# Kernel optimization log

Measured on AMD Instinct MI355X. Metric: run time of the kernel, lower is better.

The kernel has to match this reference:

```python
import jax, jax.numpy as jnp
import numpy as np

N_NODES = 100000


def gcn_conv(x, edge_index, edge_weight, W, b):
    """PyG GCNConv: out = D^-1/2 (A + I) D^-1/2 X W + b (self-loop weight 1)."""
    n = x.shape[0]
    src, dst = edge_index[0], edge_index[1]
    loop = jnp.arange(n)
    src_sl = jnp.concatenate([src, loop])
    dst_sl = jnp.concatenate([dst, loop])
    ew_sl = jnp.concatenate([edge_weight, jnp.ones((n,), x.dtype)])
    deg = jax.ops.segment_sum(ew_sl, dst_sl, num_segments=n)  # [N]
    dinv = jnp.where(deg > 0, jax.lax.rsqrt(deg), 0.0)
    norm = dinv[src_sl] * ew_sl * dinv[dst_sl]  # [E+N]
    h = x @ W  # [N, out_dim] dense transform before propagation
    msg = h[src_sl] * norm[:, None]  # gather + scale, [E+N, out_dim]
    out = jax.ops.segment_sum(msg, dst_sl, num_segments=n)  # scatter-add
    return out + b


def setup_inputs() -> dict:
    key = jax.random.key(0)
    ks = jax.random.split(key, 9)
    in_dim, hidden, latent = 128, 64, 32
    n, e = N_NODES, 1600000
    x = jax.random.normal(ks[0], (n, in_dim), dtype=jnp.float32)
    edge_index = jax.random.randint(ks[1], (2, e), 0, n, dtype=jnp.int64)
    edge_weight = jax.random.uniform(ks[2], (e,), dtype=jnp.float32)
    def glorot(k, fan_in, fan_out):
        s = jnp.sqrt(6.0 / (fan_in + fan_out))
        return jax.random.uniform(k, (fan_in, fan_out), jnp.float32, -s, s)
    return {
        "x": x,
        "edge_index": edge_index,
        "edge_weight": edge_weight,
        "W1": glorot(ks[3], in_dim, hidden),
        "b1": jnp.zeros((hidden,), jnp.float32),
        "W_mu": glorot(ks[4], hidden, latent),
        "b_mu": jnp.zeros((latent,), jnp.float32),
        "W_lv": glorot(ks[5], hidden, latent),
        "b_lv": jnp.zeros((latent,), jnp.float32),
    }


def reference(x, edge_index, edge_weight, W1, b1, W_mu, b_mu, W_lv, b_lv):
    h = jax.nn.relu(gcn_conv(x, edge_index, edge_weight, W1, b1))
    mu = gcn_conv(h, edge_index, edge_weight, W_mu, b_mu)
    logvar = gcn_conv(h, edge_index, edge_weight, W_lv, b_lv)
    return (mu, logvar)
```

## Files before the change

kernel.cpp:

```cpp
#include <hip/hip_runtime.h>

static __device__ __forceinline__ float4 ld4(const float* p) { return *(const float4*)p; }
static __device__ __forceinline__ float b2f(unsigned short u) {
    return __uint_as_float((unsigned)u << 16);
}
static __device__ __forceinline__ float b2f_lo(unsigned u) { return __uint_as_float(u << 16); }
static __device__ __forceinline__ float b2f_hi(unsigned u) { return __uint_as_float(u & 0xFFFF0000u); }
static __device__ __forceinline__ unsigned short f2b(float f) {
    unsigned x = __float_as_uint(f);
    return (unsigned short)((x + 0x7FFFu + ((x >> 16) & 1u)) >> 16);
}
static __device__ __forceinline__ unsigned pk2(float lo, float hi) {
    return (unsigned)f2b(lo) | ((unsigned)f2b(hi) << 16);
}

typedef __attribute__((ext_vector_type(8))) short bf16x8;
typedef __attribute__((ext_vector_type(4))) float f32x4;

#define NPB 256
#define CAPE 5120



__global__ __launch_bounds__(256) void k_prep(const float* __restrict__ W1,
                                              const float* __restrict__ Wmu,
                                              const float* __restrict__ Wlv,
                                              unsigned short* __restrict__ Wf1,
                                              unsigned short* __restrict__ Wf2) {
    int tid = threadIdx.x;
    if (blockIdx.x == 0) {
        for (int idx = tid; idx < 2048; idx += 256) {
            int frag = idx >> 6, lane = idx & 63;
            int s = frag & 1, ct = (frag >> 1) & 3, kb = frag >> 3;
            int rA = lane & 15, g8 = (lane >> 4) * 8;
            int c = ct * 16 + rA;
            unsigned short* dstp = Wf1 + frag * 512 + lane * 8;
            for (int j = 0; j < 8; j++) {
                float wv = W1[(size_t)(kb * 32 + g8 + j) * 64 + c];
                unsigned short hi = f2b(wv);
                dstp[j] = (s == 0) ? hi : f2b(wv - b2f(hi));
            }
        }
    } else {
        for (int idx = tid; idx < 1024; idx += 256) {
            int frag = idx >> 6, lane = idx & 63;
            int s = frag & 1, ct = (frag >> 1) & 3, kb = frag >> 3;
            int rA = lane & 15, g8 = (lane >> 4) * 8;
            int c = ct * 16 + rA;
            int k0 = kb * 32 + g8;
            unsigned short* dstp = Wf2 + frag * 512 + lane * 8;
            for (int j = 0; j < 8; j++) {
                float wv = (c < 32) ? Wmu[(size_t)(k0 + j) * 32 + c]
                                    : Wlv[(size_t)(k0 + j) * 32 + (c - 32)];
                unsigned short hi = f2b(wv);
                dstp[j] = (s == 0) ? hi : f2b(wv - b2f(hi));
            }
        }
    }
}

static __device__ __forceinline__ void split8(const float* xv, bf16x8& ah, bf16x8& al) {
    #pragma unroll
    for (int j = 0; j < 8; j++) {
        unsigned u = __float_as_uint(xv[j]);
        float res = xv[j] - __uint_as_float(u & 0xFFFF0000u);
        ah[j] = (short)(u >> 16);
        al[j] = (short)(__float_as_uint(res) >> 16);
    }
}

__global__ __launch_bounds__(256) void k_fused1(const float* __restrict__ A,
                                                const unsigned short* __restrict__ Wf1,
                                                unsigned short* __restrict__ gout,
                                                const int* __restrict__ src,
                                                const int* __restrict__ dst,
                                                const float* __restrict__ ew,
                                                int* __restrict__ bin_cnt,
                                                unsigned long long* __restrict__ ebuf,
                                                int n, int E, int gb, int bb_cnt, int NB) {
    __shared__ int hist[512];
    __shared__ int hbase[512];
    int tid = threadIdx.x;
    int bid = blockIdx.x;

    if ((bid % 5) != 4) {
        int gi = (bid / 5) * 4 + (bid % 5);
        if (gi >= gb) return;
        int row0 = gi * 64;
        int w = tid >> 6, lane = tid & 63;
        int rA = lane & 15, g8 = (lane >> 4) * 8;
        int row = row0 + w * 16 + rA;
        const float* xr = A + (size_t)min(row, n - 1) * 128;
        f32x4 acc[4] = {{0.f,0.f,0.f,0.f},{0.f,0.f,0.f,0.f},{0.f,0.f,0.f,0.f},{0.f,0.f,0.f,0.f}};
        float4 c0 = ld4(xr + g8);
        float4 c1 = ld4(xr + g8 + 4);
        #pragma unroll
        for (int kb = 0; kb < 4; kb++) {
            float4 n0, n1;
            if (kb < 3) {
                n0 = ld4(xr + (kb + 1) * 32 + g8);
                n1 = ld4(xr + (kb + 1) * 32 + g8 + 4);
            }
            float xv[8] = {c0.x, c0.y, c0.z, c0.w, c1.x, c1.y, c1.z, c1.w};
            bf16x8 ah, al;
            split8(xv, ah, al);
            const unsigned short* wb = Wf1 + (size_t)(kb * 8) * 512 + lane * 8;
            #pragma unroll
            for (int ct = 0; ct < 4; ct++) {
                bf16x8 bh = *(const bf16x8*)(wb + (ct * 2 + 0) * 512);
                bf16x8 bl = *(const bf16x8*)(wb + (ct * 2 + 1) * 512);
                acc[ct] = __builtin_amdgcn_mfma_f32_16x16x32_bf16(ah, bh, acc[ct], 0, 0, 0);
                acc[ct] = __builtin_amdgcn_mfma_f32_16x16x32_bf16(al, bh, acc[ct], 0, 0, 0);
                acc[ct] = __builtin_amdgcn_mfma_f32_16x16x32_bf16(ah, bl, acc[ct], 0, 0, 0);
            }
            if (kb < 3) { c0 = n0; c1 = n1; }
        }
        int rbase = row0 + w * 16 + (lane >> 4) * 4;
        #pragma unroll
        for (int reg = 0; reg < 4; reg++) {
            int grow = rbase + reg;
            if (grow < n) {
                #pragma unroll
                for (int ct = 0; ct < 4; ct++)
                    gout[(size_t)grow * 64 + ct * 16 + rA] = f2b(acc[ct][reg]);
            }
        }
    } else {
        int bi = bid / 5;
        if (bi >= bb_cnt) return;
        for (int j = tid; j < NB; j += 256) hist[j] = 0;
        __syncthreads();
        int e0 = bi * 4096;
        unsigned long long pk[16]; int bb[16]; int loc[16];
        #pragma unroll
        for (int j = 0; j < 16; j++) {
            int e = e0 + j * 256 + tid;
            if (e < E) {
                int s = src[e];
                int d = dst[e];
                float w = ew[e];
                bb[j] = d >> 8;
                pk[j] = ((unsigned long long)__float_as_uint(w) << 32) |
                        (unsigned)((d & (NPB - 1)) << 17) | (unsigned)s;
                loc[j] = atomicAdd(&hist[bb[j]], 1);
            } else bb[j] = -1;
        }
        __syncthreads();
        for (int j = tid; j < NB; j += 256) hbase[j] = atomicAdd(&bin_cnt[j], hist[j]);
        __syncthreads();
        #pragma unroll
        for (int j = 0; j < 16; j++) {
            if (bb[j] >= 0)
                ebuf[(size_t)bb[j] * CAPE + hbase[bb[j]] + loc[j]] = pk[j];
        }
    }
}

__global__ __launch_bounds__(512) void k_csr_build(const unsigned long long* __restrict__ ebuf,
                                                   const int* __restrict__ bin_cnt,
                                                   int2* __restrict__ rowcnt,
                                                   float* __restrict__ dinv,
                                                   unsigned long long* __restrict__ csr,
                                                   int n) {
    __shared__ unsigned long long eL[CAPE];
    __shared__ unsigned cntL[NPB];
    __shared__ unsigned ewsL[NPB];
    __shared__ unsigned fillL[NPB];
    __shared__ int scanL[512];
    __shared__ int rowL[NPB];
    __shared__ int binbase_s;
    int b = blockIdx.x;
    int tid = threadIdx.x;
    if (tid < NPB) { cntL[tid] = 0; ewsL[tid] = 0; fillL[tid] = 0; }
    scanL[tid] = (tid < b) ? bin_cnt[tid] : 0;
    __syncthreads();
    int m = bin_cnt[b];
    const unsigned long long* eb = ebuf + (size_t)b * CAPE;
    for (int i = tid; i < m; i += 512) {
        unsigned long long pk = eb[i];
        eL[i] = pk;
        int ld = (int)((pk >> 17) & (NPB - 1));
        float w = __uint_as_float((unsigned)(pk >> 32));
        atomicAdd(&cntL[ld], 1u);
        atomicAdd(&ewsL[ld], (unsigned)(w * 16777216.0f));
    }
    __syncthreads();
    #pragma unroll
    for (int off = 256; off > 0; off >>= 1) {
        if (tid < off) scanL[tid] += scanL[tid + off];
        __syncthreads();
    }
    if (tid == 0) binbase_s = scanL[0];
    __syncthreads();
    int v = (tid < NPB) ? (int)cntL[tid] : 0;
    scanL[tid] = v;
    __syncthreads();
    #pragma unroll
    for (int off = 1; off < 512; off <<= 1) {
        int t = (tid >= off) ? scanL[tid - off] : 0;
        __syncthreads();
        scanL[tid] += t;
        __syncthreads();
    }
    if (tid < NPB) {
        int rp = binbase_s + scanL[tid] - v;
        rowL[tid] = rp;
        int node = b * NPB + tid;
        if (node < n) {
            rowcnt[node] = make_int2(rp, v);
            dinv[node] = rsqrtf(1.0f + (float)ewsL[tid] * (1.0f / 16777216.0f));
        }
    }
    __syncthreads();
    for (int i = tid; i < m; i += 512) {
        unsigned long long pk = eL[i];
        int s = (int)(pk & 0x1FFFF);
        int ld = (int)((pk >> 17) & (NPB - 1));
        int pos = rowL[ld] + (int)atomicAdd(&fillL[ld], 1u);
        csr[pos] = (unsigned long long)(unsigned)s | (pk & 0xFFFFFFFF00000000ull);
    }
}

__global__ __launch_bounds__(256) void k_gemm2(const unsigned short* __restrict__ h,
                                               const unsigned short* __restrict__ Wf2,
                                               const float* __restrict__ dinv,
                                               unsigned short* __restrict__ out, int n) {
    int tid = threadIdx.x;
    int row0 = blockIdx.x * 128;
    int w = tid >> 6, lane = tid & 63;
    int rA = lane & 15, g8 = (lane >> 4) * 8;
    int rowa = row0 + w * 16 + rA;
    int rowb = rowa + 64;
    const unsigned short* ha = h + (size_t)min(rowa, n - 1) * 64;
    const unsigned short* hb = h + (size_t)min(rowb, n - 1) * 64;
    f32x4 acc0[4] = {{0.f,0.f,0.f,0.f},{0.f,0.f,0.f,0.f},{0.f,0.f,0.f,0.f},{0.f,0.f,0.f,0.f}};
    f32x4 acc1[4] = {{0.f,0.f,0.f,0.f},{0.f,0.f,0.f,0.f},{0.f,0.f,0.f,0.f},{0.f,0.f,0.f,0.f}};
    #pragma unroll
    for (int kb = 0; kb < 2; kb++) {
        bf16x8 aA = *(const bf16x8*)(ha + kb * 32 + g8);
        bf16x8 aB = *(const bf16x8*)(hb + kb * 32 + g8);
        const unsigned short* wb = Wf2 + (size_t)(kb * 8) * 512 + lane * 8;
        #pragma unroll
        for (int ct = 0; ct < 4; ct++) {
            bf16x8 bh = *(const bf16x8*)(wb + (ct * 2 + 0) * 512);
            bf16x8 bl = *(const bf16x8*)(wb + (ct * 2 + 1) * 512);
            acc0[ct] = __builtin_amdgcn_mfma_f32_16x16x32_bf16(aA, bh, acc0[ct], 0, 0, 0);
            acc0[ct] = __builtin_amdgcn_mfma_f32_16x16x32_bf16(aA, bl, acc0[ct], 0, 0, 0);
            acc1[ct] = __builtin_amdgcn_mfma_f32_16x16x32_bf16(aB, bh, acc1[ct], 0, 0, 0);
            acc1[ct] = __builtin_amdgcn_mfma_f32_16x16x32_bf16(aB, bl, acc1[ct], 0, 0, 0);
        }
    }
    int rbase = row0 + w * 16 + (lane >> 4) * 4;
    #pragma unroll
    for (int reg = 0; reg < 4; reg++) {
        int grow = rbase + reg;
        if (grow < n) {
            float sc = dinv[grow];
            #pragma unroll
            for (int ct = 0; ct < 4; ct++)
                out[(size_t)grow * 64 + ct * 16 + rA] = f2b(acc0[ct][reg] * sc);
        }
        int grow2 = grow + 64;
        if (grow2 < n) {
            float sc = dinv[grow2];
            #pragma unroll
            for (int ct = 0; ct < 4; ct++)
                out[(size_t)grow2 * 64 + ct * 16 + rA] = f2b(acc1[ct][reg] * sc);
        }
    }
}

static __device__ __forceinline__ void acc8(float* a, uint4 r, float wt) {
    a[0] = fmaf(b2f_lo(r.x), wt, a[0]); a[1] = fmaf(b2f_hi(r.x), wt, a[1]);
    a[2] = fmaf(b2f_lo(r.y), wt, a[2]); a[3] = fmaf(b2f_hi(r.y), wt, a[3]);
    a[4] = fmaf(b2f_lo(r.z), wt, a[4]); a[5] = fmaf(b2f_hi(r.z), wt, a[5]);
    a[6] = fmaf(b2f_lo(r.w), wt, a[6]); a[7] = fmaf(b2f_hi(r.w), wt, a[7]);
}

template<bool RELU, bool SPLIT_OUT, bool DSCALE>
__global__ __launch_bounds__(256) void k_prop(const unsigned short* __restrict__ g,
                                              const int2* __restrict__ csr,
                                              const int2* __restrict__ rowcnt,
                                              const float* __restrict__ dinv,
                                              const float* __restrict__ bias0,
                                              const float* __restrict__ bias1,
                                              void* __restrict__ outv, int n) {
    int node = blockIdx.x * 4 + (threadIdx.x >> 6);
    if (node >= n) return;
    int lane = threadIdx.x & 63;
    int q = lane >> 3;
    int t = lane & 7;
    uint4 sr = *(const uint4*)(g + (size_t)node * 64 + t * 8);
    int2 rc = rowcnt[node];
    const int2* ep = csr + rc.x;
    int m = rc.y;
    float a[8] = {};
    if (m > 0 && m <= 16) {
        int e1 = q, e2 = q + 8;
        int i1 = min(e1, m - 1), i2 = min(e2, m - 1);
        int2 p1 = ep[i1];
        int2 p2 = ep[i2];
        uint4 r1 = *(const uint4*)(g + (size_t)p1.x * 64 + t * 8);
        uint4 r2 = *(const uint4*)(g + (size_t)p2.x * 64 + t * 8);
        float w1 = (e1 < m) ? __int_as_float(p1.y) : 0.f;
        float w2 = (e2 < m) ? __int_as_float(p2.y) : 0.f;
        if (DSCALE) { w1 *= dinv[p1.x]; w2 *= dinv[p2.x]; }
        acc8(a, r1, w1);
        acc8(a, r2, w2);
    } else {
        for (int e = 0; e < m; e += 32) {
            int e1 = e + q, e2 = e1 + 8, e3 = e1 + 16, e4 = e1 + 24;
            int i1 = min(e1, m - 1), i2 = min(e2, m - 1);
            int i3 = min(e3, m - 1), i4 = min(e4, m - 1);
            int2 p1 = ep[i1];
            int2 p2 = ep[i2];
            int2 p3 = ep[i3];
            int2 p4 = ep[i4];
            uint4 r1 = *(const uint4*)(g + (size_t)p1.x * 64 + t * 8);
            uint4 r2 = *(const uint4*)(g + (size_t)p2.x * 64 + t * 8);
            uint4 r3 = *(const uint4*)(g + (size_t)p3.x * 64 + t * 8);
            uint4 r4 = *(const uint4*)(g + (size_t)p4.x * 64 + t * 8);
            float w1 = (e1 < m) ? __int_as_float(p1.y) : 0.f;
            float w2 = (e2 < m) ? __int_as_float(p2.y) : 0.f;
            float w3 = (e3 < m) ? __int_as_float(p3.y) : 0.f;
            float w4 = (e4 < m) ? __int_as_float(p4.y) : 0.f;
            if (DSCALE) {
                w1 *= dinv[p1.x]; w2 *= dinv[p2.x];
                w3 *= dinv[p3.x]; w4 *= dinv[p4.x];
            }
            acc8(a, r1, w1);
            acc8(a, r2, w2);
            acc8(a, r3, w3);
            acc8(a, r4, w4);
        }
    }
    #pragma unroll
    for (int i = 0; i < 8; i++) {
        a[i] += __shfl_xor(a[i], 8);
        a[i] += __shfl_xor(a[i], 16);
        a[i] += __shfl_xor(a[i], 32);
    }
    if (q != 0) return;
    float di = dinv[node];
    float ss = DSCALE ? di : 1.f;
    a[0] += ss * b2f_lo(sr.x); a[1] += ss * b2f_hi(sr.x);
    a[2] += ss * b2f_lo(sr.y); a[3] += ss * b2f_hi(sr.y);
    a[4] += ss * b2f_lo(sr.z); a[5] += ss * b2f_hi(sr.z);
    a[6] += ss * b2f_lo(sr.w); a[7] += ss * b2f_hi(sr.w);
    #pragma unroll
    for (int i = 0; i < 8; i++) a[i] *= di;
    if (!SPLIT_OUT) {
        float4 b0 = ld4(bias0 + t * 8);
        float4 b1 = ld4(bias0 + t * 8 + 4);
        a[0] += b0.x; a[1] += b0.y; a[2] += b0.z; a[3] += b0.w;
        a[4] += b1.x; a[5] += b1.y; a[6] += b1.z; a[7] += b1.w;
        if (RELU) {
            #pragma unroll
            for (int i = 0; i < 8; i++) a[i] = fmaxf(a[i], 0.f);
        }
        uint4 u = make_uint4(pk2(a[0], a[1]), pk2(a[2], a[3]),
                             pk2(a[4], a[5]), pk2(a[6], a[7]));
        *(uint4*)((unsigned short*)outv + (size_t)node * 64 + t * 8) = u;
    } else {
        float* out = (float*)outv;
        const float* bp = (t < 4) ? (bias0 + t * 8) : (bias1 + (t - 4) * 8);
        size_t base = (t < 4) ? ((size_t)node * 32 + t * 8)
                              : ((size_t)n * 32 + (size_t)node * 32 + (t - 4) * 8);
        float4 b0 = ld4(bp);
        float4 b1 = ld4(bp + 4);
        float4 v0 = make_float4(a[0] + b0.x, a[1] + b0.y, a[2] + b0.z, a[3] + b0.w);
        float4 v1 = make_float4(a[4] + b1.x, a[5] + b1.y, a[6] + b1.z, a[7] + b1.w);
        *(float4*)&out[base] = v0;
        *(float4*)&out[base + 4] = v1;
    }
}

extern "C" void kernel_launch(void* const* d_in, const int* in_sizes, int n_in,
                              void* d_out, int out_size, void* d_ws, size_t ws_size,
                              hipStream_t stream) {
    const float* x   = (const float*)d_in[0];
    const int*   ei  = (const int*)d_in[1];
    const float* ew  = (const float*)d_in[2];
    const float* W1  = (const float*)d_in[3];
    const float* b1  = (const float*)d_in[4];
    const float* Wmu = (const float*)d_in[5];
    const float* bmu = (const float*)d_in[6];
    const float* Wlv = (const float*)d_in[7];
    const float* blv = (const float*)d_in[8];
    float* outp = (float*)d_out;

    const int n = in_sizes[0] / 128;
    const int E = in_sizes[2];
    const int* src = ei;
    const int* dst = ei + E;
    const int NB = (n + NPB - 1) / NPB;

    size_t o = 0;
    auto alloc = [&](size_t bytes) { void* p = (char*)d_ws + o; o += (bytes + 511) & ~(size_t)511; return p; };
    int*   bin_cnt  = (int*)alloc((size_t)NB * 4);
    int2*  rowcnt   = (int2*)alloc((size_t)n * 8);
    float* dinv     = (float*)alloc((size_t)n * 4);
    unsigned long long* csr  = (unsigned long long*)alloc((size_t)E * 8);
    unsigned long long* ebuf = (unsigned long long*)alloc((size_t)NB * CAPE * 8);
    unsigned short* g0 = (unsigned short*)alloc((size_t)n * 64 * 2);
    unsigned short* h  = (unsigned short*)alloc((size_t)n * 64 * 2);
    unsigned short* Wf1 = (unsigned short*)alloc(32 * 512 * 2);
    unsigned short* Wf2 = (unsigned short*)alloc(16 * 512 * 2);
    unsigned short* g2 = g0;

    const int gb = (n + 63) / 64;
    const int bb = (E + 4095) / 4096;
    const int groups = max(bb, (gb + 3) / 4);

    k_prep<<<2, 256, 0, stream>>>(W1, Wmu, Wlv, Wf1, Wf2);
    hipMemsetAsync(bin_cnt, 0, (size_t)NB * 4, stream);
    k_fused1<<<groups * 5, 256, 0, stream>>>(x, Wf1, g0, src, dst, ew,
                                             bin_cnt, ebuf, n, E, gb, bb, NB);
    k_csr_build<<<NB, 512, 0, stream>>>(ebuf, bin_cnt, rowcnt, dinv, csr, n);
    k_prop<true, false, true><<<(n + 3) / 4, 256, 0, stream>>>(g0, (const int2*)csr, rowcnt, dinv,
                                                               b1, nullptr, h, n);
    k_gemm2<<<(n + 127) / 128, 256, 0, stream>>>(h, Wf2, dinv, g2, n);
    k_prop<false, true, false><<<(n + 3) / 4, 256, 0, stream>>>(g2, (const int2*)csr, rowcnt, dinv,
                                                                bmu, blv, outp, n);
}
```

Measured before the change: 274.1 us.

## Build CSR via global atomic degree count, block scan and atomic scatter

Replaces the binned edge buffer and per-bin shared-memory CSR build with three steps. A global 64-bit atomic per edge packs each node's degree count and fixed-point weight sum into one word. A per-block scan then assigns row bases through an atomic counter. A scatter kernel places edges using atomic fill counters. The source-side dinv is folded into the stored edge weight, so the propagation kernels and gemm2 no longer load or apply dinv per neighbour. This trades shared-memory binning for uncoalesced global atomics and random CSR writes, and rows end up in arbitrary block order.

Result: slower. 393.4 us (+43.5%).

```diff
diff --git a/kernel.cpp b/kernel.cpp
--- a/kernel.cpp
+++ b/kernel.cpp
@@ -16,9 +16,6 @@
 
 typedef __attribute__((ext_vector_type(8))) short bf16x8;
 typedef __attribute__((ext_vector_type(4))) float f32x4;
-
-#define NPB 256
-#define CAPE 5120
 
 
 
@@ -72,21 +69,15 @@
 __global__ __launch_bounds__(256) void k_fused1(const float* __restrict__ A,
                                                 const unsigned short* __restrict__ Wf1,
                                                 unsigned short* __restrict__ gout,
-                                                const int* __restrict__ src,
                                                 const int* __restrict__ dst,
                                                 const float* __restrict__ ew,
-                                                int* __restrict__ bin_cnt,
-                                                unsigned long long* __restrict__ ebuf,
-                                                int n, int E, int gb, int bb_cnt, int NB) {
-    __shared__ int hist[512];
-    __shared__ int hbase[512];
+                                                unsigned long long* __restrict__ deg,
+                                                int n, int E, int gb) {
     int tid = threadIdx.x;
     int bid = blockIdx.x;
 
-    if ((bid % 5) != 4) {
-        int gi = (bid / 5) * 4 + (bid % 5);
-        if (gi >= gb) return;
-        int row0 = gi * 64;
+    if (bid < gb) {
+        int row0 = bid * 64;
         int w = tid >> 6, lane = tid & 63;
         int rA = lane & 15, g8 = (lane >> 4) * 8;
         int row = row0 + w * 16 + rA;
@@ -126,104 +117,71 @@
             }
         }
     } else {
-        int bi = bid / 5;
-        if (bi >= bb_cnt) return;
-        for (int j = tid; j < NB; j += 256) hist[j] = 0;
-        __syncthreads();
-        int e0 = bi * 4096;
-        unsigned long long pk[16]; int bb[16]; int loc[16];
+        int e0 = (bid - gb) * 4096;
         #pragma unroll
         for (int j = 0; j < 16; j++) {
             int e = e0 + j * 256 + tid;
             if (e < E) {
-                int s = src[e];
                 int d = dst[e];
-                float w = ew[e];
-                bb[j] = d >> 8;
-                pk[j] = ((unsigned long long)__float_as_uint(w) << 32) |
-                        (unsigned)((d & (NPB - 1)) << 17) | (unsigned)s;
-                loc[j] = atomicAdd(&hist[bb[j]], 1);
-            } else bb[j] = -1;
-        }
-        __syncthreads();
-        for (int j = tid; j < NB; j += 256) hbase[j] = atomicAdd(&bin_cnt[j], hist[j]);
-        __syncthreads();
-        #pragma unroll
-        for (int j = 0; j < 16; j++) {
-            if (bb[j] >= 0)
-                ebuf[(size_t)bb[j] * CAPE + hbase[bb[j]] + loc[j]] = pk[j];
-        }
-    }
-}
-
-__global__ __launch_bounds__(512) void k_csr_build(const unsigned long long* __restrict__ ebuf,
-                                                   const int* __restrict__ bin_cnt,
-                                                   int2* __restrict__ rowcnt,
-                                                   float* __restrict__ dinv,
-                                                   unsigned long long* __restrict__ csr,
-                                                   int n) {
-    __shared__ unsigned long long eL[CAPE];
-    __shared__ unsigned cntL[NPB];
-    __shared__ unsigned ewsL[NPB];
-    __shared__ unsigned fillL[NPB];
-    __shared__ int scanL[512];
-    __shared__ int rowL[NPB];
-    __shared__ int binbase_s;
-    int b = blockIdx.x;
+                unsigned wfix = (unsigned)(ew[e] * 16777216.0f);
+                atomicAdd(&deg[d], (1ull << 32) | (unsigned long long)wfix);
+            }
+        }
+    }
+}
+
+__global__ __launch_bounds__(256) void k_rowptr(const unsigned long long* __restrict__ deg,
+                                                int2* __restrict__ rowcnt,
+                                                float* __restrict__ dinv,
+                                                int* __restrict__ fill,
+                                                int* __restrict__ ctr, int n) {
+    __shared__ int scanL[256];
+    __shared__ int gbase_s;
     int tid = threadIdx.x;
-    if (tid < NPB) { cntL[tid] = 0; ewsL[tid] = 0; fillL[tid] = 0; }
-    scanL[tid] = (tid < b) ? bin_cnt[tid] : 0;
+    int node = blockIdx.x * 256 + tid;
+    unsigned long long dv = (node < n) ? deg[node] : 0ull;
+    int c = (int)(dv >> 32);
+    scanL[tid] = c;
     __syncthreads();
-    int m = bin_cnt[b];
-    const unsigned long long* eb = ebuf + (size_t)b * CAPE;
-    for (int i = tid; i < m; i += 512) {
-        unsigned long long pk = eb[i];
-        eL[i] = pk;
-        int ld = (int)((pk >> 17) & (NPB - 1));
-        float w = __uint_as_float((unsigned)(pk >> 32));
-        atomicAdd(&cntL[ld], 1u);
-        atomicAdd(&ewsL[ld], (unsigned)(w * 16777216.0f));
-    }
-    __syncthreads();
-    #pragma unroll
-    for (int off = 256; off > 0; off >>= 1) {
-        if (tid < off) scanL[tid] += scanL[tid + off];
-        __syncthreads();
-    }
-    if (tid == 0) binbase_s = scanL[0];
-    __syncthreads();
-    int v = (tid < NPB) ? (int)cntL[tid] : 0;
-    scanL[tid] = v;
-    __syncthreads();
-    #pragma unroll
-    for (int off = 1; off < 512; off <<= 1) {
+    #pragma unroll
+    for (int off = 1; off < 256; off <<= 1) {
         int t = (tid >= off) ? scanL[tid - off] : 0;
         __syncthreads();
         scanL[tid] += t;
         __syncthreads();
     }
-    if (tid < NPB) {
-        int rp = binbase_s + scanL[tid] - v;
-        rowL[tid] = rp;
-        int node = b * NPB + tid;
-        if (node < n) {
-            rowcnt[node] = make_int2(rp, v);
-            dinv[node] = rsqrtf(1.0f + (float)ewsL[tid] * (1.0f / 16777216.0f));
-        }
-    }
+    if (tid == 255) gbase_s = atomicAdd(ctr, scanL[255]);
     __syncthreads();
-    for (int i = tid; i < m; i += 512) {
-        unsigned long long pk = eL[i];
-        int s = (int)(pk & 0x1FFFF);
-        int ld = (int)((pk >> 17) & (NPB - 1));
-        int pos = rowL[ld] + (int)atomicAdd(&fillL[ld], 1u);
-        csr[pos] = (unsigned long long)(unsigned)s | (pk & 0xFFFFFFFF00000000ull);
+    if (node < n) {
+        int base = gbase_s + scanL[tid] - c;
+        rowcnt[node] = make_int2(base, c);
+        fill[node] = base;
+        dinv[node] = rsqrtf(1.0f + (float)(unsigned)(dv & 0xFFFFFFFFull) * (1.0f / 16777216.0f));
+    }
+}
+
+__global__ __launch_bounds__(256) void k_scatter(const int* __restrict__ src,
+                                                 const int* __restrict__ dst,
+                                                 const float* __restrict__ ew,
+                                                 const float* __restrict__ dinv,
+                                                 int* __restrict__ fill,
+                                                 int2* __restrict__ csr, int E) {
+    int e0 = blockIdx.x * 4096;
+    #pragma unroll
+    for (int j = 0; j < 16; j++) {
+        int e = e0 + j * 256 + threadIdx.x;
+        if (e < E) {
+            int s = src[e];
+            int d = dst[e];
+            float wsc = ew[e] * dinv[s];
+            int pos = atomicAdd(&fill[d], 1);
+            csr[pos] = make_int2(s, __float_as_int(wsc));
+        }
     }
 }
 
 __global__ __launch_bounds__(256) void k_gemm2(const unsigned short* __restrict__ h,
                                                const unsigned short* __restrict__ Wf2,
-                                               const float* __restrict__ dinv,
                                                unsigned short* __restrict__ out, int n) {
     int tid = threadIdx.x;
     int row0 = blockIdx.x * 128;
@@ -255,17 +213,15 @@
     for (int reg = 0; reg < 4; reg++) {
         int grow = rbase + reg;
         if (grow < n) {
-            float sc = dinv[grow];
             #pragma unroll
             for (int ct = 0; ct < 4; ct++)
-                out[(size_t)grow * 64 + ct * 16 + rA] = f2b(acc0[ct][reg] * sc);
+                out[(size_t)grow * 64 + ct * 16 + rA] = f2b(acc0[ct][reg]);
         }
         int grow2 = grow + 64;
         if (grow2 < n) {
-            float sc = dinv[grow2];
             #pragma unroll
             for (int ct = 0; ct < 4; ct++)
-                out[(size_t)grow2 * 64 + ct * 16 + rA] = f2b(acc1[ct][reg] * sc);
+                out[(size_t)grow2 * 64 + ct * 16 + rA] = f2b(acc1[ct][reg]);
         }
     }
 }
@@ -277,7 +233,7 @@
     a[6] = fmaf(b2f_lo(r.w), wt, a[6]); a[7] = fmaf(b2f_hi(r.w), wt, a[7]);
 }
 
-template<bool RELU, bool SPLIT_OUT, bool DSCALE>
+template<bool RELU, bool SPLIT_OUT>
 __global__ __launch_bounds__(256) void k_prop(const unsigned short* __restrict__ g,
                                               const int2* __restrict__ csr,
                                               const int2* __restrict__ rowcnt,
@@ -304,7 +260,6 @@
         uint4 r2 = *(const uint4*)(g + (size_t)p2.x * 64 + t * 8);
         float w1 = (e1 < m) ? __int_as_float(p1.y) : 0.f;
         float w2 = (e2 < m) ? __int_as_float(p2.y) : 0.f;
-        if (DSCALE) { w1 *= dinv[p1.x]; w2 *= dinv[p2.x]; }
         acc8(a, r1, w1);
         acc8(a, r2, w2);
     } else {
@@ -324,10 +279,6 @@
             float w2 = (e2 < m) ? __int_as_float(p2.y) : 0.f;
             float w3 = (e3 < m) ? __int_as_float(p3.y) : 0.f;
             float w4 = (e4 < m) ? __int_as_float(p4.y) : 0.f;
-            if (DSCALE) {
-                w1 *= dinv[p1.x]; w2 *= dinv[p2.x];
-                w3 *= dinv[p3.x]; w4 *= dinv[p4.x];
-            }
             acc8(a, r1, w1);
             acc8(a, r2, w2);
             acc8(a, r3, w3);
@@ -342,11 +293,10 @@
     }
     if (q != 0) return;
     float di = dinv[node];
-    float ss = DSCALE ? di : 1.f;
-    a[0] += ss * b2f_lo(sr.x); a[1] += ss * b2f_hi(sr.x);
-    a[2] += ss * b2f_lo(sr.y); a[3] += ss * b2f_hi(sr.y);
-    a[4] += ss * b2f_lo(sr.z); a[5] += ss * b2f_hi(sr.z);
-    a[6] += ss * b2f_lo(sr.w); a[7] += ss * b2f_hi(sr.w);
+    a[0] += di * b2f_lo(sr.x); a[1] += di * b2f_hi(sr.x);
+    a[2] += di * b2f_lo(sr.y); a[3] += di * b2f_hi(sr.y);
+    a[4] += di * b2f_lo(sr.z); a[5] += di * b2f_hi(sr.z);
+    a[6] += di * b2f_lo(sr.w); a[7] += di * b2f_hi(sr.w);
     #pragma unroll
     for (int i = 0; i < 8; i++) a[i] *= di;
     if (!SPLIT_OUT) {
@@ -393,15 +343,15 @@
     const int E = in_sizes[2];
     const int* src = ei;
     const int* dst = ei + E;
-    const int NB = (n + NPB - 1) / NPB;
 
     size_t o = 0;
     auto alloc = [&](size_t bytes) { void* p = (char*)d_ws + o; o += (bytes + 511) & ~(size_t)511; return p; };
-    int*   bin_cnt  = (int*)alloc((size_t)NB * 4);
+    unsigned long long* deg = (unsigned long long*)alloc((size_t)n * 8);
     int2*  rowcnt   = (int2*)alloc((size_t)n * 8);
     float* dinv     = (float*)alloc((size_t)n * 4);
-    unsigned long long* csr  = (unsigned long long*)alloc((size_t)E * 8);
-    unsigned long long* ebuf = (unsigned long long*)alloc((size_t)NB * CAPE * 8);
+    int*   fill     = (int*)alloc((size_t)n * 4);
+    int*   ctr      = (int*)alloc(512);
+    int2*  csr      = (int2*)alloc((size_t)E * 8);
     unsigned short* g0 = (unsigned short*)alloc((size_t)n * 64 * 2);
     unsigned short* h  = (unsigned short*)alloc((size_t)n * 64 * 2);
     unsigned short* Wf1 = (unsigned short*)alloc(32 * 512 * 2);
@@ -410,16 +360,17 @@
 
     const int gb = (n + 63) / 64;
     const int bb = (E + 4095) / 4096;
-    const int groups = max(bb, (gb + 3) / 4);
+    const int nbq = (n + 255) / 256;
 
     k_prep<<<2, 256, 0, stream>>>(W1, Wmu, Wlv, Wf1, Wf2);
-    hipMemsetAsync(bin_cnt, 0, (size_t)NB * 4, stream);
-    k_fused1<<<groups * 5, 256, 0, stream>>>(x, Wf1, g0, src, dst, ew,
-                                             bin_cnt, ebuf, n, E, gb, bb, NB);
-    k_csr_build<<<NB, 512, 0, stream>>>(ebuf, bin_cnt, rowcnt, dinv, csr, n);
-    k_prop<true, false, true><<<(n + 3) / 4, 256, 0, stream>>>(g0, (const int2*)csr, rowcnt, dinv,
-                                                               b1, nullptr, h, n);
-    k_gemm2<<<(n + 127) / 128, 256, 0, stream>>>(h, Wf2, dinv, g2, n);
-    k_prop<false, true, false><<<(n + 3) / 4, 256, 0, stream>>>(g2, (const int2*)csr, rowcnt, dinv,
-                                                                bmu, blv, outp, n);
-}
+    hipMemsetAsync(deg, 0, (size_t)n * 8, stream);
+    hipMemsetAsync(ctr, 0, 4, stream);
+    k_fused1<<<gb + bb, 256, 0, stream>>>(x, Wf1, g0, dst, ew, deg, n, E, gb);
+    k_rowptr<<<nbq, 256, 0, stream>>>(deg, rowcnt, dinv, fill, ctr, n);
+    k_scatter<<<bb, 256, 0, stream>>>(src, dst, ew, dinv, fill, csr, E);
+    k_prop<true, false><<<(n + 3) / 4, 256, 0, stream>>>(g0, csr, rowcnt, dinv,
+                                                         b1, nullptr, h, n);
+    k_gemm2<<<(n + 127) / 128, 256, 0, stream>>>(h, Wf2, g2, n);
+    k_prop<false, true><<<(n + 3) / 4, 256, 0, stream>>>(g2, csr, rowcnt, dinv,
+                                                         bmu, blv, outp, n);
+}
```

## Shrink CSR bins to 64 nodes and add separate bin-offset scan kernel

Applied to the files above, without the earlier changes.

Cuts nodes per bin from 256 to 64, which gives about 1563 bins with a 1536-entry capacity each. The per-block prefix over earlier bins in the CSR builder is replaced by a dedicated single-block scan kernel. The fused GEMM/binning kernel changes from interleaved 4:1 block assignment to contiguous GEMM blocks followed by binning blocks. The goal is more, smaller CSR-build blocks with less LDS and a cheaper per-block scan, so occupancy and parallelism go up. The cost is a larger shared histogram (1600 entries) in the binning blocks, more global atomics into bin_cnt, and one extra kernel launch.

After: 276.0 us. No clear change (+0.7%).

```diff
diff --git a/kernel.cpp b/kernel.cpp
--- a/kernel.cpp
+++ b/kernel.cpp
@@ -17,8 +17,9 @@
 typedef __attribute__((ext_vector_type(8))) short bf16x8;
 typedef __attribute__((ext_vector_type(4))) float f32x4;
 
-#define NPB 256
-#define CAPE 5120
+#define NPB 64
+#define CAPE 1536
+#define NBMAX 1600
 
 
 
@@ -77,16 +78,14 @@
                                                 const float* __restrict__ ew,
                                                 int* __restrict__ bin_cnt,
                                                 unsigned long long* __restrict__ ebuf,
-                                                int n, int E, int gb, int bb_cnt, int NB) {
-    __shared__ int hist[512];
-    __shared__ int hbase[512];
+                                                int n, int E, int gb, int NB) {
+    __shared__ int hist[NBMAX];
+    __shared__ int hbase[NBMAX];
     int tid = threadIdx.x;
     int bid = blockIdx.x;
 
-    if ((bid % 5) != 4) {
-        int gi = (bid / 5) * 4 + (bid % 5);
-        if (gi >= gb) return;
-        int row0 = gi * 64;
+    if (bid < gb) {
+        int row0 = bid * 64;
         int w = tid >> 6, lane = tid & 63;
         int rA = lane & 15, g8 = (lane >> 4) * 8;
         int row = row0 + w * 16 + rA;
@@ -126,11 +125,9 @@
             }
         }
     } else {
-        int bi = bid / 5;
-        if (bi >= bb_cnt) return;
         for (int j = tid; j < NB; j += 256) hist[j] = 0;
         __syncthreads();
-        int e0 = bi * 4096;
+        int e0 = (bid - gb) * 4096;
         unsigned long long pk[16]; int bb[16]; int loc[16];
         #pragma unroll
         for (int j = 0; j < 16; j++) {
@@ -139,7 +136,7 @@
                 int s = src[e];
                 int d = dst[e];
                 float w = ew[e];
-                bb[j] = d >> 8;
+                bb[j] = d >> 6;
                 pk[j] = ((unsigned long long)__float_as_uint(w) << 32) |
                         (unsigned)((d & (NPB - 1)) << 17) | (unsigned)s;
                 loc[j] = atomicAdd(&hist[bb[j]], 1);
@@ -156,27 +153,57 @@
     }
 }
 
-__global__ __launch_bounds__(512) void k_csr_build(const unsigned long long* __restrict__ ebuf,
+__global__ __launch_bounds__(256) void k_binscan(const int* __restrict__ bin_cnt,
+                                                 int* __restrict__ bin_base, int NB) {
+    __shared__ int sums[256];
+    int tid = threadIdx.x;
+    int per = (NB + 255) / 256;
+    int start = tid * per;
+    int loc[8];
+    int s = 0;
+    for (int i = 0; i < per; i++) {
+        int idx = start + i;
+        int v = (idx < NB) ? bin_cnt[idx] : 0;
+        loc[i] = s;
+        s += v;
+    }
+    sums[tid] = s;
+    __syncthreads();
+    #pragma unroll
+    for (int off = 1; off < 256; off <<= 1) {
+        int t = (tid >= off) ? sums[tid - off] : 0;
+        __syncthreads();
+        sums[tid] += t;
+        __syncthreads();
+    }
+    int base = (tid > 0) ? sums[tid - 1] : 0;
+    for (int i = 0; i < per; i++) {
+        int idx = start + i;
+        if (idx < NB) bin_base[idx] = base + loc[i];
+    }
+}
+
+__global__ __launch_bounds__(256) void k_csr_build(const unsigned long long* __restrict__ ebuf,
                                                    const int* __restrict__ bin_cnt,
+                                                   const int* __restrict__ bin_base,
                                                    int2* __restrict__ rowcnt,
                                                    float* __restrict__ dinv,
-                                                   unsigned long long* __restrict__ csr,
+                                                   int2* __restrict__ csr,
                                                    int n) {
     __shared__ unsigned long long eL[CAPE];
     __shared__ unsigned cntL[NPB];
     __shared__ unsigned ewsL[NPB];
     __shared__ unsigned fillL[NPB];
-    __shared__ int scanL[512];
+    __shared__ int scanL[NPB];
     __shared__ int rowL[NPB];
-    __shared__ int binbase_s;
     int b = blockIdx.x;
     int tid = threadIdx.x;
     if (tid < NPB) { cntL[tid] = 0; ewsL[tid] = 0; fillL[tid] = 0; }
-    scanL[tid] = (tid < b) ? bin_cnt[tid] : 0;
     __syncthreads();
     int m = bin_cnt[b];
+    int base = bin_base[b];
     const unsigned long long* eb = ebuf + (size_t)b * CAPE;
-    for (int i = tid; i < m; i += 512) {
+    for (int i = tid; i < m; i += 256) {
         unsigned long long pk = eb[i];
         eL[i] = pk;
         int ld = (int)((pk >> 17) & (NPB - 1));
@@ -185,25 +212,18 @@
         atomicAdd(&ewsL[ld], (unsigned)(w * 16777216.0f));
     }
     __syncthreads();
-    #pragma unroll
-    for (int off = 256; off > 0; off >>= 1) {
-        if (tid < off) scanL[tid] += scanL[tid + off];
-        __syncthreads();
-    }
-    if (tid == 0) binbase_s = scanL[0];
+    if (tid < NPB) scanL[tid] = (int)cntL[tid];
     __syncthreads();
-    int v = (tid < NPB) ? (int)cntL[tid] : 0;
-    scanL[tid] = v;
-    __syncthreads();
-    #pragma unroll
-    for (int off = 1; off < 512; off <<= 1) {
-        int t = (tid >= off) ? scanL[tid - off] : 0;
-        __syncthreads();
-        scanL[tid] += t;
+    #pragma unroll
+    for (int off = 1; off < NPB; off <<= 1) {
+        int t = (tid < NPB && tid >= off) ? scanL[tid - off] : 0;
+        __syncthreads();
+        if (tid < NPB) scanL[tid] += t;
         __syncthreads();
     }
     if (tid < NPB) {
-        int rp = binbase_s + scanL[tid] - v;
+        int v = (int)cntL[tid];
+        int rp = base + scanL[tid] - v;
         rowL[tid] = rp;
         int node = b * NPB + tid;
         if (node < n) {
@@ -212,12 +232,12 @@
         }
     }
     __syncthreads();
-    for (int i = tid; i < m; i += 512) {
+    for (int i = tid; i < m; i += 256) {
         unsigned long long pk = eL[i];
         int s = (int)(pk & 0x1FFFF);
         int ld = (int)((pk >> 17) & (NPB - 1));
         int pos = rowL[ld] + (int)atomicAdd(&fillL[ld], 1u);
-        csr[pos] = (unsigned long long)(unsigned)s | (pk & 0xFFFFFFFF00000000ull);
+        csr[pos] = make_int2(s, (int)(pk >> 32));
     }
 }
 
@@ -398,9 +418,10 @@
     size_t o = 0;
     auto alloc = [&](size_t bytes) { void* p = (char*)d_ws + o; o += (bytes + 511) & ~(size_t)511; return p; };
     int*   bin_cnt  = (int*)alloc((size_t)NB * 4);
+    int*   bin_base = (int*)alloc((size_t)NB * 4);
     int2*  rowcnt   = (int2*)alloc((size_t)n * 8);
     float* dinv     = (float*)alloc((size_t)n * 4);
-    unsigned long long* csr  = (unsigned long long*)alloc((size_t)E * 8);
+    int2*  csr      = (int2*)alloc((size_t)E * 8);
     unsigned long long* ebuf = (unsigned long long*)alloc((size_t)NB * CAPE * 8);
     unsigned short* g0 = (unsigned short*)alloc((size_t)n * 64 * 2);
     unsigned short* h  = (unsigned short*)alloc((size_t)n * 64 * 2);
@@ -410,16 +431,16 @@
 
     const int gb = (n + 63) / 64;
     const int bb = (E + 4095) / 4096;
-    const int groups = max(bb, (gb + 3) / 4);
 
     k_prep<<<2, 256, 0, stream>>>(W1, Wmu, Wlv, Wf1, Wf2);
     hipMemsetAsync(bin_cnt, 0, (size_t)NB * 4, stream);
-    k_fused1<<<groups * 5, 256, 0, stream>>>(x, Wf1, g0, src, dst, ew,
-                                             bin_cnt, ebuf, n, E, gb, bb, NB);
-    k_csr_build<<<NB, 512, 0, stream>>>(ebuf, bin_cnt, rowcnt, dinv, csr, n);
-    k_prop<true, false, true><<<(n + 3) / 4, 256, 0, stream>>>(g0, (const int2*)csr, rowcnt, dinv,
+    k_fused1<<<gb + bb, 256, 0, stream>>>(x, Wf1, g0, src, dst, ew,
+                                          bin_cnt, ebuf, n, E, gb, NB);
+    k_binscan<<<1, 256, 0, stream>>>(bin_cnt, bin_base, NB);
+    k_csr_build<<<NB, 256, 0, stream>>>(ebuf, bin_cnt, bin_base, rowcnt, dinv, csr, n);
+    k_prop<true, false, true><<<(n + 3) / 4, 256, 0, stream>>>(g0, csr, rowcnt, dinv,
                                                                b1, nullptr, h, n);
     k_gemm2<<<(n + 127) / 128, 256, 0, stream>>>(h, Wf2, dinv, g2, n);
-    k_prop<false, true, false><<<(n + 3) / 4, 256, 0, stream>>>(g2, (const int2*)csr, rowcnt, dinv,
+    k_prop<false, true, false><<<(n + 3) / 4, 256, 0, stream>>>(g2, csr, rowcnt, dinv,
                                                                 bmu, blv, outp, n);
 }
```
